# Performance work log

Measured on AMD Instinct MI355X. Metric: run time of the kernel, lower is better.

The kernel has to match this reference:

```python
import jax, jax.numpy as jnp
import numpy as np

N_NODES = 50000
N_EDGES = 800000
DIM = 128
LN_EPS = 1e-5


def setup_inputs() -> dict:
    key = jax.random.key(0)
    k1, k2, k3, k4, k5 = jax.random.split(key, 5)
    x = jax.random.normal(k1, (N_NODES, DIM), dtype=jnp.float32)
    edge_index = jax.random.randint(k2, (2, N_EDGES), 0, N_NODES, dtype=jnp.int64)
    edge_weight = jax.random.uniform(k3, (N_EDGES,), dtype=jnp.float32)
    # GCNConv linear (PyG Linear: out = x @ W.T + b)
    W = jax.random.normal(k4, (DIM, DIM), dtype=jnp.float32) / np.sqrt(DIM)
    b = jnp.zeros((DIM,), dtype=jnp.float32)
    # pygnn.LayerNorm(dim, mode='node') affine params
    ln_weight = jnp.ones((DIM,), dtype=jnp.float32)
    ln_bias = jnp.zeros((DIM,), dtype=jnp.float32)
    return {"x": x, "edge_index": edge_index, "edge_weight": edge_weight,
            "W": W, "b": b, "ln_weight": ln_weight, "ln_bias": ln_bias}


def reference(x, edge_index, edge_weight, W, b, ln_weight, ln_bias):
    n = x.shape[0]
    # --- LayerNorm (mode='node'): per-node over feature dim ---
    mu = jnp.mean(x, axis=-1, keepdims=True)
    var = jnp.mean(jnp.square(x - mu), axis=-1, keepdims=True)
    xn = (x - mu) * jax.lax.rsqrt(var + LN_EPS) * ln_weight + ln_bias
    # --- GCNConv: linear first, then normalized propagate ---
    h = xn @ W.T  # [N, dim]
    row, col = edge_index[0], edge_index[1]  # source, target
    # add self loops (fill_value = 1.0)
    loop = jnp.arange(n, dtype=edge_index.dtype)
    row_f = jnp.concatenate([row, loop])
    col_f = jnp.concatenate([col, loop])
    ew_f = jnp.concatenate([edge_weight, jnp.ones((n,), dtype=edge_weight.dtype)])
    # symmetric gcn normalization: deg over target (col)
    deg = jax.ops.segment_sum(ew_f, col_f, num_segments=n)
    dinv = jnp.where(deg > 0, jax.lax.rsqrt(deg), 0.0)
    norm = dinv[row_f] * ew_f * dinv[col_f]  # [E+N]
    # gather-scale-scatter
    msg = h[row_f] * norm[:, None]  # [E+N, dim]
    out = jax.ops.segment_sum(msg, col_f, num_segments=n) + b
    # --- GELU (torch default = exact erf form); dropout is identity (p=0 / eval) ---
    return jax.nn.gelu(out, approximate=False)
```

## Files before the change

kernel.cpp:

```cpp
#include <hip/hip_runtime.h>
#include <math.h>

#define DIM 128
#define LN_EPS 1e-5f
#define HB 512
#define CAP 2048

typedef __attribute__((ext_vector_type(8))) short short8;
typedef __attribute__((ext_vector_type(4))) float floatx4;

__device__ __forceinline__ float gelu_exact(float v) {
    return 0.5f * v * (1.0f + erff(v * 0.70710678118654752f));
}
__device__ __forceinline__ float bf2f(unsigned short u) {
    return __uint_as_float(((unsigned)u) << 16);
}
__device__ __forceinline__ short f2bf(float f) {
    unsigned b = __float_as_uint(f);
    return (short)((b + 0x7FFF + ((b >> 16) & 1)) >> 16);
}

__global__ __launch_bounds__(256) void wconv_kernel(
    const float* __restrict__ W, short* __restrict__ wfrag)
{
    int c = blockIdx.x * 256 + threadIdx.x;
    int nrow = ((c >> 8) << 4) | (c & 15);
    int kb   = (((c >> 6) & 3) << 5) + (((c >> 4) & 3) << 3);
    const float* wp = W + nrow * DIM + kb;
    float4 w0 = *(const float4*)wp;
    float4 w1 = *(const float4*)(wp + 4);
    short8 p;
    p[0] = f2bf(w0.x); p[1] = f2bf(w0.y); p[2] = f2bf(w0.z); p[3] = f2bf(w0.w);
    p[4] = f2bf(w1.x); p[5] = f2bf(w1.y); p[6] = f2bf(w1.z); p[7] = f2bf(w1.w);
    *(short8*)&wfrag[c * 8] = p;
}

__global__ __launch_bounds__(256) void gemm_hist_kernel(
    const float* __restrict__ x, const short* __restrict__ wfrag,
    const float* __restrict__ lnw, const float* __restrict__ lnb,
    unsigned short* __restrict__ h16,
    const int* __restrict__ col, int* __restrict__ hist,
    int n, int E, int nbkt)
{
    __shared__ short ubuf[8448];
    const int tid = threadIdx.x;

    if ((int)blockIdx.x < HB) {
        int* lh = (int*)ubuf;
        for (int b = tid; b < nbkt; b += 256) lh[b] = 0;
        __syncthreads();
        int g = blockIdx.x;
        int chunk = (E + HB - 1) / HB;
        int e0 = g * chunk;
        int e1 = e0 + chunk; if (e1 > E) e1 = E;
        for (int e = e0 + tid; e < e1; e += 256)
            atomicAdd(&lh[col[e] >> 6], 1);
        __syncthreads();
        for (int b = tid; b < nbkt; b += 256)
            hist[(size_t)g * nbkt + b] = lh[b];
        return;
    }

    const int gb = blockIdx.x - HB;
    const int n0 = gb * 64;
    short* axb = ubuf;

    {
        int m = tid >> 2, sub = tid & 3;
        int node = n0 + m;
        bool valid = (node < n);
        const float4* xp = (const float4*)(x + (size_t)node * DIM + sub * 32);
        float4 v[8];
        float s = 0.f, ss = 0.f;
        #pragma unroll
        for (int i = 0; i < 8; ++i) {
            v[i] = valid ? xp[i] : make_float4(0.f, 0.f, 0.f, 0.f);
            s  += v[i].x + v[i].y + v[i].z + v[i].w;
            ss += v[i].x * v[i].x + v[i].y * v[i].y + v[i].z * v[i].z + v[i].w * v[i].w;
        }
        s += __shfl_xor(s, 1); ss += __shfl_xor(ss, 1);
        s += __shfl_xor(s, 2); ss += __shfl_xor(ss, 2);
        float mu   = s * (1.0f / 128.0f);
        float var  = ss * (1.0f / 128.0f) - mu * mu;
        float rstd = rsqrtf(var + LN_EPS);

        int mt = m >> 4, mloc = m & 15;
        #pragma unroll
        for (int quad = 0; quad < 4; ++quad) {
            float4 a = v[2 * quad], c4 = v[2 * quad + 1];
            const float4* lw = (const float4*)(lnw + sub * 32 + quad * 8);
            const float4* lb = (const float4*)(lnb + sub * 32 + quad * 8);
            float4 lw0 = lw[0], lw1 = lw[1], lb0 = lb[0], lb1 = lb[1];
            short8 p;
            p[0] = f2bf((a.x  - mu) * rstd * lw0.x + lb0.x);
            p[1] = f2bf((a.y  - mu) * rstd * lw0.y + lb0.y);
            p[2] = f2bf((a.z  - mu) * rstd * lw0.z + lb0.z);
            p[3] = f2bf((a.w  - mu) * rstd * lw0.w + lb0.w);
            p[4] = f2bf((c4.x - mu) * rstd * lw1.x + lb1.x);
            p[5] = f2bf((c4.y - mu) * rstd * lw1.y + lb1.y);
            p[6] = f2bf((c4.z - mu) * rstd * lw1.z + lb1.z);
            p[7] = f2bf((c4.w - mu) * rstd * lw1.w + lb1.w);
            int slot = mt * 256 + sub * 64 + quad * 16 + mloc;
            *(short8*)&axb[slot * 8] = p;
        }
    }
    __syncthreads();

    const int w    = tid >> 6;
    const int lane = tid & 63;
    const short8* wf = (const short8*)wfrag;

    short8 afrag[4];
    #pragma unroll
    for (int kq = 0; kq < 4; ++kq)
        afrag[kq] = *(const short8*)&axb[(w * 256 + kq * 64 + lane) * 8];
    __syncthreads();

    floatx4 acc[8];
    #pragma unroll
    for (int jt = 0; jt < 8; ++jt) acc[jt] = (floatx4){0.f, 0.f, 0.f, 0.f};

    #pragma unroll
    for (int jt = 0; jt < 8; ++jt) {
        #pragma unroll
        for (int kq = 0; kq < 4; ++kq) {
            short8 bfrag = wf[jt * 256 + kq * 64 + lane];
            acc[jt] = __builtin_amdgcn_mfma_f32_16x16x32_bf16(afrag[kq], bfrag,
                                                              acc[jt], 0, 0, 0);
        }
    }

    const int quad = lane >> 4, nl = lane & 15;
    const int HS = 132;
    short* hb = ubuf;
    #pragma unroll
    for (int jt = 0; jt < 8; ++jt) {
        #pragma unroll
        for (int r = 0; r < 4; ++r)
            hb[(w * 16 + quad * 4 + r) * HS + jt * 16 + nl] = f2bf(acc[jt][r]);
    }
    __syncthreads();
    {
        int rrow = tid >> 2, seg = tid & 3;
        int node = n0 + rrow;
        if (node < n) {
            const short8* sp = (const short8*)&hb[rrow * HS + seg * 32];
            short8 v0 = sp[0], v1 = sp[1], v2 = sp[2], v3 = sp[3];
            short8* dp = (short8*)(h16 + (size_t)node * DIM + seg * 32);
            dp[0] = v0; dp[1] = v1; dp[2] = v2; dp[3] = v3;
        }
    }
}

__global__ __launch_bounds__(256) void expand_kernel(
    const int* __restrict__ hist, int* __restrict__ base,
    int* __restrict__ cnt, int nbkt)
{
    __shared__ int ls[256];
    const int tid = threadIdx.x;
    const int b = blockIdx.x;

    int v0 = hist[(size_t)(2 * tid)     * nbkt + b];
    int v1 = hist[(size_t)(2 * tid + 1) * nbkt + b];
    int p = v0 + v1;
    ls[tid] = p;
    __syncthreads();
    int inc = p;
    for (int off = 1; off < 256; off <<= 1) {
        int add = (tid >= off) ? ls[tid - off] : 0;
        __syncthreads();
        inc += add;
        ls[tid] = inc;
        __syncthreads();
    }
    int ex = inc - p;
    int a0 = b * CAP + ex;
    base[(size_t)(2 * tid)     * nbkt + b] = a0;
    base[(size_t)(2 * tid + 1) * nbkt + b] = a0 + v0;
    if (tid == 255) cnt[b] = inc;
}

__global__ __launch_bounds__(256) void bucket_scatter_kernel(
    const int* __restrict__ row, const int* __restrict__ col,
    const float* __restrict__ ew, const int* __restrict__ base,
    int2* __restrict__ srt, int E, int nbkt)
{
    __shared__ int cur[1024];
    const int tid = threadIdx.x, g = blockIdx.x;
    for (int b = tid; b < nbkt; b += 256)
        cur[b] = base[(size_t)g * nbkt + b];
    __syncthreads();
    int chunk = (E + HB - 1) / HB;
    int e0 = g * chunk;
    int e1 = e0 + chunk; if (e1 > E) e1 = E;
    for (int e = e0 + tid; e < e1; e += 256) {
        int c = col[e];
        int pos = atomicAdd(&cur[c >> 6], 1);
        srt[pos] = make_int2(((c & 63) << 16) | row[e], __float_as_int(ew[e]));
    }
}

__global__ __launch_bounds__(256) void dinv_kernel(
    const int2* __restrict__ srt, const int* __restrict__ cnt,
    float* __restrict__ dinv, int n)
{
    __shared__ float w64[64];
    const int tid = threadIdx.x, b = blockIdx.x;
    if (tid < 64) w64[tid] = 0.f;
    __syncthreads();
    int c = cnt[b];
    int s0 = b * CAP;
    for (int i = tid; i < c; i += 256) {
        int2 v = srt[s0 + i];
        atomicAdd(&w64[(v.x >> 16) & 63], __int_as_float(v.y));
    }
    __syncthreads();
    if (tid < 64)
        dinv[b * 64 + tid] = rsqrtf(1.0f + w64[tid]);
}

__global__ __launch_bounds__(256) void bucket_gather_kernel(
    const int2* __restrict__ srt, const int* __restrict__ cnt,
    const float* __restrict__ dinv, const unsigned short* __restrict__ h16,
    const float* __restrict__ bias, float* __restrict__ out, int n)
{
    __shared__ int2  bufA[CAP];
    __shared__ int2  bufB[CAP];
    __shared__ int   k64[64], off64[64], cur64[64];
    __shared__ float di64[64];
    const int tid = threadIdx.x, b = blockIdx.x;

    if (tid < 64) { k64[tid] = 0; di64[tid] = dinv[b * 64 + tid]; }
    __syncthreads();

    const int c  = cnt[b];
    const int s0 = b * CAP;
    const int grp = tid >> 4;
    const int sub = tid & 15;

    if (c <= CAP) {
        for (int i = tid; i < c; i += 256) {
            int2 v = srt[s0 + i];
            bufA[i] = v;
            atomicAdd(&k64[(v.x >> 16) & 63], 1);
        }
        __syncthreads();
        if (tid == 0) {
            int run = 0;
            #pragma unroll
            for (int d = 0; d < 64; ++d) { off64[d] = run; cur64[d] = run; run += k64[d]; }
        }
        __syncthreads();
        for (int i = tid; i < c; i += 256) {
            int2 v = bufA[i];
            int d   = (v.x >> 16) & 63;
            int src = v.x & 0xFFFF;
            float nrm = dinv[src] * __int_as_float(v.y) * di64[d];
            int p = atomicAdd(&cur64[d], 1);
            bufB[p] = make_int2(src, __float_as_int(nrm));
        }
        __syncthreads();

        #pragma unroll
        for (int dd = 0; dd < 4; ++dd) {
            int d = dd * 16 + grp;
            int dest = b * 64 + d;
            if (dest >= n) continue;
            float di = di64[d];
            short8 sv = *(const short8*)(h16 + (size_t)dest * DIM + sub * 8);
            float s2 = di * di;
            float acc[8];
            #pragma unroll
            for (int k = 0; k < 8; ++k) acc[k] = s2 * bf2f((unsigned short)sv[k]);

            int j  = off64[d];
            int je = j + k64[d];
            for (; j + 3 < je; j += 4) {
                int2 e0 = bufB[j],     e1 = bufB[j + 1];
                int2 e2 = bufB[j + 2], e3 = bufB[j + 3];
                short8 a0 = *(const short8*)(h16 + (size_t)e0.x * DIM + sub * 8);
                short8 a1 = *(const short8*)(h16 + (size_t)e1.x * DIM + sub * 8);
                short8 a2 = *(const short8*)(h16 + (size_t)e2.x * DIM + sub * 8);
                short8 a3 = *(const short8*)(h16 + (size_t)e3.x * DIM + sub * 8);
                float n0 = __int_as_float(e0.y);
                float n1 = __int_as_float(e1.y);
                float n2 = __int_as_float(e2.y);
                float n3 = __int_as_float(e3.y);
                #pragma unroll
                for (int k = 0; k < 8; ++k) {
                    acc[k] = fmaf(n0, bf2f((unsigned short)a0[k]), acc[k]);
                    acc[k] = fmaf(n1, bf2f((unsigned short)a1[k]), acc[k]);
                    acc[k] = fmaf(n2, bf2f((unsigned short)a2[k]), acc[k]);
                    acc[k] = fmaf(n3, bf2f((unsigned short)a3[k]), acc[k]);
                }
            }
            for (; j < je; ++j) {
                int2 e0 = bufB[j];
                float n0 = __int_as_float(e0.y);
                short8 a = *(const short8*)(h16 + (size_t)e0.x * DIM + sub * 8);
                #pragma unroll
                for (int k = 0; k < 8; ++k)
                    acc[k] = fmaf(n0, bf2f((unsigned short)a[k]), acc[k]);
            }

            float4 b0 = *(const float4*)(bias + sub * 8);
            float4 b1 = *(const float4*)(bias + sub * 8 + 4);
            float4 o0, o1;
            o0.x = gelu_exact(acc[0] + b0.x); o0.y = gelu_exact(acc[1] + b0.y);
            o0.z = gelu_exact(acc[2] + b0.z); o0.w = gelu_exact(acc[3] + b0.w);
            o1.x = gelu_exact(acc[4] + b1.x); o1.y = gelu_exact(acc[5] + b1.y);
            o1.z = gelu_exact(acc[6] + b1.z); o1.w = gelu_exact(acc[7] + b1.w);
            float* op = out + (size_t)dest * DIM + sub * 8;
            *(float4*)op       = o0;
            *(float4*)(op + 4) = o1;
        }
    } else {
        #pragma unroll
        for (int dd = 0; dd < 4; ++dd) {
            int d = dd * 16 + grp;
            int dest = b * 64 + d;
            if (dest >= n) continue;
            float di = di64[d];
            short8 sv = *(const short8*)(h16 + (size_t)dest * DIM + sub * 8);
            float s2 = di * di;
            float acc[8];
            #pragma unroll
            for (int k = 0; k < 8; ++k) acc[k] = s2 * bf2f((unsigned short)sv[k]);
            for (int i = 0; i < c; ++i) {
                int2 v = srt[s0 + i];
                if (((v.x >> 16) & 63) != d) continue;
                int src = v.x & 0xFFFF;
                float nrm = dinv[src] * __int_as_float(v.y) * di;
                short8 a = *(const short8*)(h16 + (size_t)src * DIM + sub * 8);
                #pragma unroll
                for (int k = 0; k < 8; ++k)
                    acc[k] = fmaf(nrm, bf2f((unsigned short)a[k]), acc[k]);
            }
            float4 b0 = *(const float4*)(bias + sub * 8);
            float4 b1 = *(const float4*)(bias + sub * 8 + 4);
            float4 o0, o1;
            o0.x = gelu_exact(acc[0] + b0.x); o0.y = gelu_exact(acc[1] + b0.y);
            o0.z = gelu_exact(acc[2] + b0.z); o0.w = gelu_exact(acc[3] + b0.w);
            o1.x = gelu_exact(acc[4] + b1.x); o1.y = gelu_exact(acc[5] + b1.y);
            o1.z = gelu_exact(acc[6] + b1.z); o1.w = gelu_exact(acc[7] + b1.w);
            float* op = out + (size_t)dest * DIM + sub * 8;
            *(float4*)op       = o0;
            *(float4*)(op + 4) = o1;
        }
    }
}

extern "C" void kernel_launch(void* const* d_in, const int* in_sizes, int n_in,
                              void* d_out, int out_size, void* d_ws, size_t ws_size,
                              hipStream_t stream)
{
    const float* x    = (const float*)d_in[0];
    const int*   ei   = (const int*)d_in[1];
    const float* ew   = (const float*)d_in[2];
    const float* W    = (const float*)d_in[3];
    const float* b    = (const float*)d_in[4];
    const float* ln_w = (const float*)d_in[5];
    const float* ln_b = (const float*)d_in[6];
    float* out = (float*)d_out;

    const int n = in_sizes[0] / DIM;
    const int E = in_sizes[2];
    const int* row  = ei;
    const int* colp = ei + E;
    const int nbkt = (n + 63) / 64;

    int2*           srt   = (int2*)d_ws;
    unsigned short* h16   = (unsigned short*)(srt + (size_t)nbkt * CAP);
    short*          wfrag = (short*)(h16 + (size_t)n * DIM);
    int*            hist  = (int*)(wfrag + 16384);
    int*            base  = hist + (size_t)HB * nbkt;
    int*            cnt   = base + (size_t)HB * nbkt;
    float*          dinv  = (float*)(cnt + nbkt);

    const int GB = (n + 63) / 64;

    wconv_kernel<<<8, 256, 0, stream>>>(W, wfrag);
    gemm_hist_kernel<<<HB + GB, 256, 0, stream>>>(x, wfrag, ln_w, ln_b, h16,
                                                  colp, hist, n, E, nbkt);
    expand_kernel<<<nbkt, 256, 0, stream>>>(hist, base, cnt, nbkt);
    bucket_scatter_kernel<<<HB, 256, 0, stream>>>(row, colp, ew, base, srt, E, nbkt);
    dinv_kernel<<<nbkt, 256, 0, stream>>>(srt, cnt, dinv, n);
    bucket_gather_kernel<<<nbkt, 256, 0, stream>>>(srt, cnt, dinv, h16, b, out, n);
}
```

Before: 173.7 us.

## Replace histogram-scan bucketing with global atomic cursors and fold W conversion into GEMM

New measurement: 346.0 us. +99.2%, slower.

```diff
diff --git a/kernel.cpp b/kernel.cpp
--- a/kernel.cpp
+++ b/kernel.cpp
@@ -3,7 +3,6 @@
 
 #define DIM 128
 #define LN_EPS 1e-5f
-#define HB 512
 #define CAP 2048
 
 typedef __attribute__((ext_vector_type(8))) short short8;
@@ -20,50 +19,31 @@
     return (short)((b + 0x7FFF + ((b >> 16) & 1)) >> 16);
 }
 
-__global__ __launch_bounds__(256) void wconv_kernel(
-    const float* __restrict__ W, short* __restrict__ wfrag)
-{
-    int c = blockIdx.x * 256 + threadIdx.x;
-    int nrow = ((c >> 8) << 4) | (c & 15);
-    int kb   = (((c >> 6) & 3) << 5) + (((c >> 4) & 3) << 3);
-    const float* wp = W + nrow * DIM + kb;
-    float4 w0 = *(const float4*)wp;
-    float4 w1 = *(const float4*)(wp + 4);
-    short8 p;
-    p[0] = f2bf(w0.x); p[1] = f2bf(w0.y); p[2] = f2bf(w0.z); p[3] = f2bf(w0.w);
-    p[4] = f2bf(w1.x); p[5] = f2bf(w1.y); p[6] = f2bf(w1.z); p[7] = f2bf(w1.w);
-    *(short8*)&wfrag[c * 8] = p;
-}
-
-__global__ __launch_bounds__(256) void gemm_hist_kernel(
-    const float* __restrict__ x, const short* __restrict__ wfrag,
+__global__ __launch_bounds__(256) void gemm_kernel(
+    const float* __restrict__ x, const float* __restrict__ W,
     const float* __restrict__ lnw, const float* __restrict__ lnb,
-    unsigned short* __restrict__ h16,
-    const int* __restrict__ col, int* __restrict__ hist,
-    int n, int E, int nbkt)
-{
+    unsigned short* __restrict__ h16, int* __restrict__ cursor, int n)
+{
+    __shared__ short swb[2048 * 8];
     __shared__ short ubuf[8448];
     const int tid = threadIdx.x;
-
-    if ((int)blockIdx.x < HB) {
-        int* lh = (int*)ubuf;
-        for (int b = tid; b < nbkt; b += 256) lh[b] = 0;
-        __syncthreads();
-        int g = blockIdx.x;
-        int chunk = (E + HB - 1) / HB;
-        int e0 = g * chunk;
-        int e1 = e0 + chunk; if (e1 > E) e1 = E;
-        for (int e = e0 + tid; e < e1; e += 256)
-            atomicAdd(&lh[col[e] >> 6], 1);
-        __syncthreads();
-        for (int b = tid; b < nbkt; b += 256)
-            hist[(size_t)g * nbkt + b] = lh[b];
-        return;
-    }
-
-    const int gb = blockIdx.x - HB;
+    const int gb = blockIdx.x;
     const int n0 = gb * 64;
     short* axb = ubuf;
+
+    if (tid == 0) cursor[gb] = gb * CAP;
+
+    for (int c = tid; c < 2048; c += 256) {
+        int nrow = ((c >> 8) << 4) | (c & 15);
+        int kb   = (((c >> 6) & 3) << 5) + (((c >> 4) & 3) << 3);
+        const float* wp = W + nrow * DIM + kb;
+        float4 w0 = *(const float4*)wp;
+        float4 w1 = *(const float4*)(wp + 4);
+        short8 p;
+        p[0] = f2bf(w0.x); p[1] = f2bf(w0.y); p[2] = f2bf(w0.z); p[3] = f2bf(w0.w);
+        p[4] = f2bf(w1.x); p[5] = f2bf(w1.y); p[6] = f2bf(w1.z); p[7] = f2bf(w1.w);
+        *(short8*)&swb[c * 8] = p;
+    }
 
     {
         int m = tid >> 2, sub = tid & 3;
@@ -108,7 +88,6 @@
 
     const int w    = tid >> 6;
     const int lane = tid & 63;
-    const short8* wf = (const short8*)wfrag;
 
     short8 afrag[4];
     #pragma unroll
@@ -124,7 +103,7 @@
     for (int jt = 0; jt < 8; ++jt) {
         #pragma unroll
         for (int kq = 0; kq < 4; ++kq) {
-            short8 bfrag = wf[jt * 256 + kq * 64 + lane];
+            short8 bfrag = *(const short8*)&swb[(jt * 256 + kq * 64 + lane) * 8];
             acc[jt] = __builtin_amdgcn_mfma_f32_16x16x32_bf16(afrag[kq], bfrag,
                                                               acc[jt], 0, 0, 0);
         }
@@ -152,63 +131,29 @@
     }
 }
 
-__global__ __launch_bounds__(256) void expand_kernel(
-    const int* __restrict__ hist, int* __restrict__ base,
-    int* __restrict__ cnt, int nbkt)
-{
-    __shared__ int ls[256];
-    const int tid = threadIdx.x;
-    const int b = blockIdx.x;
-
-    int v0 = hist[(size_t)(2 * tid)     * nbkt + b];
-    int v1 = hist[(size_t)(2 * tid + 1) * nbkt + b];
-    int p = v0 + v1;
-    ls[tid] = p;
-    __syncthreads();
-    int inc = p;
-    for (int off = 1; off < 256; off <<= 1) {
-        int add = (tid >= off) ? ls[tid - off] : 0;
-        __syncthreads();
-        inc += add;
-        ls[tid] = inc;
-        __syncthreads();
-    }
-    int ex = inc - p;
-    int a0 = b * CAP + ex;
-    base[(size_t)(2 * tid)     * nbkt + b] = a0;
-    base[(size_t)(2 * tid + 1) * nbkt + b] = a0 + v0;
-    if (tid == 255) cnt[b] = inc;
-}
-
-__global__ __launch_bounds__(256) void bucket_scatter_kernel(
+__global__ __launch_bounds__(256) void scatter_atomic_kernel(
     const int* __restrict__ row, const int* __restrict__ col,
-    const float* __restrict__ ew, const int* __restrict__ base,
-    int2* __restrict__ srt, int E, int nbkt)
-{
-    __shared__ int cur[1024];
-    const int tid = threadIdx.x, g = blockIdx.x;
-    for (int b = tid; b < nbkt; b += 256)
-        cur[b] = base[(size_t)g * nbkt + b];
-    __syncthreads();
-    int chunk = (E + HB - 1) / HB;
-    int e0 = g * chunk;
-    int e1 = e0 + chunk; if (e1 > E) e1 = E;
-    for (int e = e0 + tid; e < e1; e += 256) {
+    const float* __restrict__ ew, int* __restrict__ cursor,
+    int2* __restrict__ srt, int E)
+{
+    int e = blockIdx.x * 256 + threadIdx.x;
+    int stride = gridDim.x * 256;
+    for (; e < E; e += stride) {
         int c = col[e];
-        int pos = atomicAdd(&cur[c >> 6], 1);
+        int pos = atomicAdd(&cursor[c >> 6], 1);
         srt[pos] = make_int2(((c & 63) << 16) | row[e], __float_as_int(ew[e]));
     }
 }
 
 __global__ __launch_bounds__(256) void dinv_kernel(
-    const int2* __restrict__ srt, const int* __restrict__ cnt,
+    const int2* __restrict__ srt, const int* __restrict__ cursor,
     float* __restrict__ dinv, int n)
 {
     __shared__ float w64[64];
     const int tid = threadIdx.x, b = blockIdx.x;
     if (tid < 64) w64[tid] = 0.f;
     __syncthreads();
-    int c = cnt[b];
+    int c = cursor[b] - b * CAP;
     int s0 = b * CAP;
     for (int i = tid; i < c; i += 256) {
         int2 v = srt[s0 + i];
@@ -220,7 +165,7 @@
 }
 
 __global__ __launch_bounds__(256) void bucket_gather_kernel(
-    const int2* __restrict__ srt, const int* __restrict__ cnt,
+    const int2* __restrict__ srt, const int* __restrict__ cursor,
     const float* __restrict__ dinv, const unsigned short* __restrict__ h16,
     const float* __restrict__ bias, float* __restrict__ out, int n)
 {
@@ -233,7 +178,7 @@
     if (tid < 64) { k64[tid] = 0; di64[tid] = dinv[b * 64 + tid]; }
     __syncthreads();
 
-    const int c  = cnt[b];
+    const int c  = cursor[b] - b * CAP;
     const int s0 = b * CAP;
     const int grp = tid >> 4;
     const int sub = tid & 15;
@@ -245,10 +190,16 @@
             atomicAdd(&k64[(v.x >> 16) & 63], 1);
         }
         __syncthreads();
-        if (tid == 0) {
-            int run = 0;
+        if (tid < 64) {
+            int v = k64[tid];
+            int inc = v;
             #pragma unroll
-            for (int d = 0; d < 64; ++d) { off64[d] = run; cur64[d] = run; run += k64[d]; }
+            for (int off = 1; off < 64; off <<= 1) {
+                int t = __shfl_up(inc, off, 64);
+                if (tid >= off) inc += t;
+            }
+            off64[tid] = inc - v;
+            cur64[tid] = inc - v;
         }
         __syncthreads();
         for (int i = tid; i < c; i += 256) {
@@ -369,21 +320,20 @@
     const int* colp = ei + E;
     const int nbkt = (n + 63) / 64;
 
-    int2*           srt   = (int2*)d_ws;
-    unsigned short* h16   = (unsigned short*)(srt + (size_t)nbkt * CAP);
-    short*          wfrag = (short*)(h16 + (size_t)n * DIM);
-    int*            hist  = (int*)(wfrag + 16384);
-    int*            base  = hist + (size_t)HB * nbkt;
-    int*            cnt   = base + (size_t)HB * nbkt;
-    float*          dinv  = (float*)(cnt + nbkt);
+    int2*           srt    = (int2*)d_ws;
+    unsigned short* h16    = (unsigned short*)(srt + (size_t)nbkt * CAP);
+    int*            cursor = (int*)(h16 + (size_t)n * DIM);
+    float*          dinv   = (float*)(cursor + nbkt);
 
     const int GB = (n + 63) / 64;
 
-    wconv_kernel<<<8, 256, 0, stream>>>(W, wfrag);
-    gemm_hist_kernel<<<HB + GB, 256, 0, stream>>>(x, wfrag, ln_w, ln_b, h16,
-                                                  colp, hist, n, E, nbkt);
-    expand_kernel<<<nbkt, 256, 0, stream>>>(hist, base, cnt, nbkt);
-    bucket_scatter_kernel<<<HB, 256, 0, stream>>>(row, colp, ew, base, srt, E, nbkt);
-    dinv_kernel<<<nbkt, 256, 0, stream>>>(srt, cnt, dinv, n);
-    bucket_gather_kernel<<<nbkt, 256, 0, stream>>>(srt, cnt, dinv, h16, b, out, n);
-}
+    gemm_kernel<<<GB, 256, 0, stream>>>(x, W, ln_w, ln_b, h16, cursor, n);
+    {
+        int blocks = (E + 255) / 256;
+        if (blocks > 2048) blocks = 2048;
+        scatter_atomic_kernel<<<blocks, 256, 0, stream>>>(row, colp, ew,
+                                                          cursor, srt, E);
+    }
+    dinv_kernel<<<nbkt, 256, 0, stream>>>(srt, cursor, dinv, n);
+    bucket_gather_kernel<<<nbkt, 256, 0, stream>>>(srt, cursor, dinv, h16, b, out, n);
+}
```
